# Kernel optimization log

Hardware: AMD Instinct MI355X
Metric: run time of the kernel (lower is better)

Reference implementation:

```python
import jax, jax.numpy as jnp
import numpy as np

B, N, T, E = 8, 4096, 16, 65536
D, H, O = 768, 4, 256
PER_TURN = N // T
NEG = -1e30


def setup_inputs() -> dict:
    key = jax.random.key(0)
    k = jax.random.split(key, 10)
    x = jax.random.normal(k[0], (B, N, D), dtype=jnp.float32)
    # turns sorted within each graph: node i has turn i // PER_TURN
    turns = jnp.tile(jnp.repeat(jnp.arange(T, dtype=jnp.int32), PER_TURN)[None, :], (B, 1))
    # edges: dst uniform over nodes, src uniform over nodes with turn[src] <= turn[dst]
    dst = jax.random.randint(k[1], (B, E), 0, N, dtype=jnp.int32)
    bound = (dst // PER_TURN + 1) * PER_TURN
    u = jax.random.uniform(k[2], (B, E), dtype=jnp.float32)
    src = jnp.minimum((u * bound).astype(jnp.int32), bound - 1)
    edge_index = jnp.stack([src, dst], axis=1)  # [B, 2, E]
    W = jax.random.normal(k[3], (D, H * D), dtype=jnp.float32) * 0.02
    a_src = jax.random.normal(k[4], (H, D), dtype=jnp.float32) * 0.05
    a_dst = jax.random.normal(k[5], (H, D), dtype=jnp.float32) * 0.05
    b_gat = jnp.zeros((D,), jnp.float32)
    w_att = jax.random.normal(k[6], (D, 1), dtype=jnp.float32) * 0.05
    b_att = jnp.zeros((1,), jnp.float32)
    w_cls = jax.random.normal(k[7], (D, O), dtype=jnp.float32) * 0.05
    b_cls = jnp.zeros((O,), jnp.float32)
    return dict(x=x, edge_index=edge_index, turns=turns, W=W, a_src=a_src,
                a_dst=a_dst, b_gat=b_gat, w_att=w_att, b_att=b_att,
                w_cls=w_cls, b_cls=b_cls)


def _forward(x, edge_index, turns, W, a_src, a_dst, b_gat, w_att, b_att, w_cls, b_cls, n_turns):
    n = x.shape[1]
    h_heads, d = a_src.shape

    def graph_fn(args):
        xg, ei, tg = args
        src, dst = ei[0], ei[1]

        def step(xc, t):
            active = tg <= t                                  # subgraph node mask [N]
            h = (xc @ W).reshape(n, h_heads, d)               # [N,H,D] per-head projections
            asrc = jnp.einsum('nhd,hd->nh', h, a_src)         # [N,H]
            adst = jnp.einsum('nhd,hd->nh', h, a_dst)
            emask = tg[dst] == t                              # only edges into current turn
            e = jax.nn.leaky_relu(asrc[src] + adst[dst], 0.2)  # [E,H]
            e = jnp.where(emask[:, None], e, NEG)
            # PyG GATConv add_self_loops=True: self-loop on every subgraph node
            s = jax.nn.leaky_relu(asrc + adst, 0.2)           # [N,H]
            s = jnp.where(active[:, None], s, NEG)
            m = jnp.maximum(jax.ops.segment_max(e, dst, num_segments=n), s)
            m = jnp.where(m > NEG * 0.5, m, 0.0)              # safe max for empty segments
            ee = jnp.where(emask[:, None], jnp.exp(e - m[dst]), 0.0)   # [E,H]
            se = jnp.where(active[:, None], jnp.exp(s - m), 0.0)       # [N,H]
            denom = jax.ops.segment_sum(ee, dst, num_segments=n) + se  # [N,H]
            msg = jax.ops.segment_sum(ee[:, :, None] * h[src], dst, num_segments=n)
            out = (msg + se[:, :, None] * h) / jnp.where(denom > 0, denom, 1.0)[:, :, None]
            out = out.mean(axis=1) + b_gat                    # concat=False -> mean over heads
            xn = jnp.where(active[:, None], out, xc)          # write back into graph.x
            # GlobalAttention pooling over subgraph nodes
            gate = (xn @ w_att + b_att).squeeze(-1)           # [N]
            g = jax.nn.softmax(jnp.where(active, gate, NEG))
            pooled = g @ xn                                   # [D]
            return xn, pooled @ w_cls + b_cls                 # [O]

        _, outs = jax.lax.scan(step, xg, jnp.arange(n_turns))
        return outs                                           # [T,O]

    outs = jax.lax.map(graph_fn, (x, edge_index, turns))      # sequential over graphs
    return outs[:, :, None, :]                                # [B,T,1,O] like torch.stack nesting


def reference(x, edge_index, turns, W, a_src, a_dst, b_gat, w_att, b_att, w_cls, b_cls):
    n_turns = int(turns.max()) + 1
    return _forward(x, edge_index, turns, W, a_src, a_dst, b_gat, w_att, b_att,
                    w_cls, b_cls, n_turns)
```

## Files before the change

kernel.cpp:

```cpp
#include <hip/hip_runtime.h>

typedef __attribute__((ext_vector_type(8))) short short8;
typedef __attribute__((ext_vector_type(8))) unsigned short ushort8;
typedef __attribute__((ext_vector_type(4))) float f32x4;

__device__ __forceinline__ float b2f(unsigned short u){
  union { unsigned int i; float f; } v; v.i = ((unsigned int)u)<<16; return v.f;
}
__device__ __forceinline__ unsigned short f2b(float f){
  unsigned int x = __float_as_uint(f);
  return (unsigned short)((x + 0x7fffu + ((x>>16)&1u))>>16);
}

__device__ __forceinline__ void gload16(const unsigned short* g, unsigned short* l){
  __builtin_amdgcn_global_load_lds((const __attribute__((address_space(1))) unsigned int*)g,
                                   (__attribute__((address_space(3))) unsigned int*)l, 16, 0, 0);
}

__global__ __launch_bounds__(256) void k_zero(int* p){
  p[blockIdx.x*256 + threadIdx.x] = 0;
}

__global__ __launch_bounds__(256) void k_hist(const int* __restrict__ ei, int* __restrict__ cnt){
  int idx = blockIdx.x*256 + threadIdx.x;
  int b = idx>>16, e = idx&65535;
  int dst = ei[b*131072 + 65536 + e];
  atomicAdd(&cnt[b*4096 + dst], 1);
}

__global__ __launch_bounds__(1024) void k_scan(int* __restrict__ cnt, int* __restrict__ offs){
  int b = blockIdx.x, tid = threadIdx.x;
  __shared__ int sums[1024];
  int base = tid*4;
  int c0 = cnt[b*4096+base+0], c1 = cnt[b*4096+base+1];
  int c2 = cnt[b*4096+base+2], c3 = cnt[b*4096+base+3];
  int t1 = c0, t2 = c0+c1, t3 = c0+c1+c2, tot = t3+c3;
  sums[tid] = tot;
  __syncthreads();
  for (int off=1; off<1024; off<<=1){
    int add = (tid>=off) ? sums[tid-off] : 0;
    __syncthreads();
    sums[tid] += add;
    __syncthreads();
  }
  int eb = sums[tid] - tot;
  offs[b*4097+base+0] = eb;      offs[b*4097+base+1] = eb+t1;
  offs[b*4097+base+2] = eb+t2;   offs[b*4097+base+3] = eb+t3;
  cnt[b*4096+base+0] = eb;       cnt[b*4096+base+1] = eb+t1;
  cnt[b*4096+base+2] = eb+t2;    cnt[b*4096+base+3] = eb+t3;
  if (tid==1023) offs[b*4097+4096] = sums[1023];
}

__global__ __launch_bounds__(256) void k_scatter(const int* __restrict__ ei, int* __restrict__ cur,
                                                 int* __restrict__ ss){
  int idx = blockIdx.x*256 + threadIdx.x;
  int b = idx>>16, e = idx&65535;
  int src = ei[b*131072 + e];
  int dst = ei[b*131072 + 65536 + e];
  int pos = atomicAdd(&cur[b*4096 + dst], 1);
  ss[b*65536 + pos] = src;
}

__global__ __launch_bounds__(256) void k_vavd(const float* __restrict__ W, const float* __restrict__ a_src,
                                              const float* __restrict__ a_dst, float* __restrict__ vavd){
  int wid = blockIdx.x*4 + (threadIdx.x>>6);
  int lane = threadIdx.x & 63;
  int i = wid>>3, h8 = wid&7, h = h8&3;
  const float* a = (h8<4 ? a_src : a_dst) + h*768;
  const float* wrow = W + i*3072 + h*768;
  float acc = 0.f;
  #pragma unroll
  for (int j12=0; j12<12; j12++){ int j = lane + j12*64; acc += wrow[j]*a[j]; }
  #pragma unroll
  for (int d=1; d<64; d<<=1) acc += __shfl_xor(acc, d);
  if (lane==0) vavd[i*8 + h8] = acc;
}

__global__ __launch_bounds__(256) void k_prep_w(const float* __restrict__ W, unsigned short* __restrict__ wmT,
                                                unsigned short* __restrict__ wpT){
  int g = blockIdx.x*256 + threadIdx.x;
  int i = g%768, j = g/768;
  float s = 0.f;
  #pragma unroll
  for (int h=0; h<4; h++){
    float w = W[i*3072 + h*768 + j];
    s += w;
    wpT[j*3072 + h*768 + i] = f2b(w);
  }
  wmT[j*768 + i] = f2b(0.25f*s);
}

__global__ __launch_bounds__(256) void k_prep0(const float* __restrict__ x0, const float* __restrict__ vavd,
                                               float* __restrict__ ad0){
  int b = blockIdx.y;
  int node = blockIdx.x*4 + (threadIdx.x>>6);
  int lane = threadIdx.x & 63;
  size_t roff = (size_t)(b*4096 + node)*768;
  float acc[8];
  #pragma unroll
  for (int k=0;k<8;k++) acc[k]=0.f;
  #pragma unroll
  for (int j12=0; j12<12; j12++){
    int j = lane + j12*64;
    float xv = x0[roff + j];
    const float* vp = vavd + j*8;
    #pragma unroll
    for (int k=0;k<8;k++) acc[k]+=xv*vp[k];
  }
  #pragma unroll
  for (int k=0;k<8;k++){
    #pragma unroll
    for (int d=1; d<64; d<<=1) acc[k] += __shfl_xor(acc[k], d);
  }
  if (lane==0){
    float* o = ad0 + (size_t)(b*4096 + node)*8;
    #pragma unroll
    for (int k=0;k<8;k++) o[k]=acc[k];
  }
}

__global__ __launch_bounds__(256) void k_edge(const float* __restrict__ x0, const unsigned short* __restrict__ stc,
                                              const float* __restrict__ ad, const float* __restrict__ ad0,
                                              const int* __restrict__ offs,
                                              const int* __restrict__ ssrc, unsigned short* __restrict__ zbuf, int t){
  int b = blockIdx.y, dl = blockIdx.x, tid = threadIdx.x;
  int dst = t*256 + dl;
  int lane = tid&63, wv = tid>>6;
  int e0 = offs[b*4097 + dst], e1 = offs[b*4097 + dst + 1];
  const float* adr = ad0 + (size_t)(b*4096 + dst)*8;
  float ad0_=adr[4], ad1_=adr[5], ad2_=adr[6], ad3_=adr[7];
  float sh[4];
  { float v;
    v=adr[0]+ad0_; sh[0]=v>0.f?v:0.2f*v;
    v=adr[1]+ad1_; sh[1]=v>0.f?v:0.2f*v;
    v=adr[2]+ad2_; sh[2]=v>0.f?v:0.2f*v;
    v=adr[3]+ad3_; sh[3]=v>0.f?v:0.2f*v; }
  int band = t*256;
  float mx[4] = {-1e30f,-1e30f,-1e30f,-1e30f};
  for (int i=e0+tid; i<e1; i+=256){
    int s = ssrc[b*65536 + i];
    const float* ap = (s >= band ? ad0 : ad) + (size_t)(b*4096 + s)*8;
    float v;
    v=ap[0]+ad0_; v=v>0.f?v:0.2f*v; mx[0]=fmaxf(mx[0],v);
    v=ap[1]+ad1_; v=v>0.f?v:0.2f*v; mx[1]=fmaxf(mx[1],v);
    v=ap[2]+ad2_; v=v>0.f?v:0.2f*v; mx[2]=fmaxf(mx[2],v);
    v=ap[3]+ad3_; v=v>0.f?v:0.2f*v; mx[3]=fmaxf(mx[3],v);
  }
  #pragma unroll
  for (int h=0;h<4;h++){
    #pragma unroll
    for (int d=1; d<64; d<<=1) mx[h] = fmaxf(mx[h], __shfl_xor(mx[h], d));
  }
  __shared__ float redm[4][4];
  if (lane==0){ redm[wv][0]=mx[0]; redm[wv][1]=mx[1]; redm[wv][2]=mx[2]; redm[wv][3]=mx[3]; }
  __syncthreads();
  float m[4];
  #pragma unroll
  for (int h=0;h<4;h++)
    m[h] = fmaxf(fmaxf(fmaxf(redm[0][h],redm[1][h]),fmaxf(redm[2][h],redm[3][h])), sh[h]);

  __shared__ float4 eeL[256];
  __shared__ int srcL[256];
  float den0=0.f,den1=0.f,den2=0.f,den3=0.f;
  float za[4][3] = {{0,0,0},{0,0,0},{0,0,0},{0,0,0}};
  for (int base=e0; base<e1; base+=256){
    __syncthreads();
    int i = base + tid;
    if (i < e1){
      int s = ssrc[b*65536 + i];
      const float* ap = (s >= band ? ad0 : ad) + (size_t)(b*4096 + s)*8;
      float4 wq; float v;
      v=ap[0]+ad0_; v=v>0.f?v:0.2f*v; wq.x=expf(v-m[0]); den0+=wq.x;
      v=ap[1]+ad1_; v=v>0.f?v:0.2f*v; wq.y=expf(v-m[1]); den1+=wq.y;
      v=ap[2]+ad2_; v=v>0.f?v:0.2f*v; wq.z=expf(v-m[2]); den2+=wq.z;
      v=ap[3]+ad3_; v=v>0.f?v:0.2f*v; wq.w=expf(v-m[3]); den3+=wq.w;
      eeL[tid] = wq; srcL[tid] = s;
    }
    __syncthreads();
    int cnt = e1 - base; if (cnt > 256) cnt = 256;
    for (int k=0; k<cnt; k++){
      float4 wq = eeL[k];
      int s = srcL[k];
      float xv0, xv1, xv2;
      if (s < band){
        const unsigned short* r = stc + (size_t)(b*4096 + s)*768;
        xv0=b2f(r[tid]); xv1=b2f(r[tid+256]); xv2=b2f(r[tid+512]);
      } else {
        const float* r = x0 + (size_t)(b*4096 + s)*768;
        xv0=r[tid]; xv1=r[tid+256]; xv2=r[tid+512];
      }
      za[0][0]+=wq.x*xv0; za[0][1]+=wq.x*xv1; za[0][2]+=wq.x*xv2;
      za[1][0]+=wq.y*xv0; za[1][1]+=wq.y*xv1; za[1][2]+=wq.y*xv2;
      za[2][0]+=wq.z*xv0; za[2][1]+=wq.z*xv1; za[2][2]+=wq.z*xv2;
      za[3][0]+=wq.w*xv0; za[3][1]+=wq.w*xv1; za[3][2]+=wq.w*xv2;
    }
  }
  float se[4];
  #pragma unroll
  for (int h=0;h<4;h++) se[h] = expf(sh[h]-m[h]);
  { const float* r = x0 + (size_t)(b*4096 + dst)*768;
    float xv0=r[tid], xv1=r[tid+256], xv2=r[tid+512];
    za[0][0]+=se[0]*xv0; za[0][1]+=se[0]*xv1; za[0][2]+=se[0]*xv2;
    za[1][0]+=se[1]*xv0; za[1][1]+=se[1]*xv1; za[1][2]+=se[1]*xv2;
    za[2][0]+=se[2]*xv0; za[2][1]+=se[2]*xv1; za[2][2]+=se[2]*xv2;
    za[3][0]+=se[3]*xv0; za[3][1]+=se[3]*xv1; za[3][2]+=se[3]*xv2; }
  float den[4]={den0,den1,den2,den3};
  #pragma unroll
  for (int h=0;h<4;h++){
    #pragma unroll
    for (int d=1; d<64; d<<=1) den[h] += __shfl_xor(den[h], d);
  }
  __shared__ float redd[4][4];
  if (lane==0){ redd[wv][0]=den[0]; redd[wv][1]=den[1]; redd[wv][2]=den[2]; redd[wv][3]=den[3]; }
  __syncthreads();
  unsigned short* zp = zbuf + (size_t)(b*256 + dl)*3072;
  #pragma unroll
  for (int h=0;h<4;h++){
    float dtot = redd[0][h]+redd[1][h]+redd[2][h]+redd[3][h] + se[h];
    float sc = 0.25f/dtot;
    zp[h*768 + tid      ] = f2b(za[h][0]*sc);
    zp[h*768 + tid + 256] = f2b(za[h][1]*sc);
    zp[h*768 + tid + 512] = f2b(za[h][2]*sc);
  }
}

__global__ __launch_bounds__(512) void k_mm(const unsigned short* __restrict__ zbuf,
                                            const unsigned short* __restrict__ wpT,
                                            const unsigned short* __restrict__ stc,
                                            const unsigned short* __restrict__ wmT,
                                            const float* __restrict__ bias,
                                            unsigned short* __restrict__ partA,
                                            unsigned short* __restrict__ stn, int t){
  int nwg = gridDim.x, orig = blockIdx.x;
  int cpx = nwg>>3;
  int j = (orig&7)*cpx + (orig>>3);

  int tid = threadIdx.x, lane = tid&63, w = tid>>6;
  bool jobA = j < 192;
  const unsigned short *Ap, *Bp;
  int lda, ldb, s = 0, b = 0, mrow, ncol;
  if (jobA){
    s = j/48; int q = j%48;
    mrow = (q/6)*256; ncol = (q%6)*128;
    Ap = zbuf + (size_t)mrow*3072 + s*768;  lda = 3072;
    Bp = wpT  + (size_t)ncol*3072 + s*768;  ldb = 3072;
  } else {
    int idx = j - 192; int pg = 6*t;
    b = idx/pg; int rr = idx%pg;
    mrow = (rr/6)*256; ncol = (rr%6)*128;
    Ap = stc + (size_t)b*4096*768 + (size_t)mrow*768;  lda = 768;
    Bp = wmT + (size_t)ncol*768;                       ldb = 768;
  }
  int wr = (w>>1)*64, wc = (w&1)*64;
  int lrow = lane&15, lk = (lane>>4)*8;
  __shared__ unsigned short As[3][256*32];
  __shared__ unsigned short Bs[3][128*32];
  f32x4 acc[4][4];
  #pragma unroll
  for (int m=0;m<4;m++)
    #pragma unroll
    for (int n2=0;n2<4;n2++) acc[m][n2] = (f32x4){0.f,0.f,0.f,0.f};
  int srow = w*16 + (lane>>2);
  int skb  = (lane&3)*8;
  const unsigned short* ga0 = Ap + (size_t)srow*lda + skb;
  const unsigned short* ga1 = Ap + (size_t)(128+srow)*lda + skb;
  const unsigned short* gb0 = Bp + (size_t)srow*ldb + skb;
  int lo = w*512;
  #define STAGE(bi) { gload16(ga0, &As[bi][lo]); gload16(ga1, &As[bi][4096+lo]); \
                      gload16(gb0, &Bs[bi][lo]); \
                      ga0 += 32; ga1 += 32; gb0 += 32; }
  STAGE(0)
  STAGE(1)
  #pragma unroll
  for (int kt=0; kt<24; kt++){
    int cur = kt%3;
    if (kt < 22) STAGE((kt+2)%3)
    if (kt < 22)      asm volatile("s_waitcnt vmcnt(6)" ::: "memory");
    else if (kt==22)  asm volatile("s_waitcnt vmcnt(3)" ::: "memory");
    else              asm volatile("s_waitcnt vmcnt(0)" ::: "memory");
    __builtin_amdgcn_sched_barrier(0);
    __builtin_amdgcn_s_barrier();
    __builtin_amdgcn_sched_barrier(0);
    short8 af[4], bf[4];
    #pragma unroll
    for (int m=0;m<4;m++)  af[m]  = *(const short8*)&As[cur][(wr + m*16 + lrow)*32 + lk];
    #pragma unroll
    for (int n2=0;n2<4;n2++) bf[n2] = *(const short8*)&Bs[cur][(wc + n2*16 + lrow)*32 + lk];
    __builtin_amdgcn_s_setprio(1);
    #pragma unroll
    for (int m=0;m<4;m++)
      #pragma unroll
      for (int n2=0;n2<4;n2++)
        acc[m][n2] = __builtin_amdgcn_mfma_f32_16x16x32_bf16(af[m], bf[n2], acc[m][n2], 0,0,0);
    __builtin_amdgcn_s_setprio(0);
    __builtin_amdgcn_sched_barrier(0);
    __builtin_amdgcn_s_barrier();
    __builtin_amdgcn_sched_barrier(0);
  }
  #undef STAGE
  if (jobA){
    unsigned short* op = partA + (size_t)s*2048*768;
    #pragma unroll
    for (int m=0;m<4;m++)
      #pragma unroll
      for (int n2=0;n2<4;n2++)
        #pragma unroll
        for (int r=0;r<4;r++){
          int gr = mrow + wr + m*16 + (lane>>4)*4 + r;
          int gc = ncol + wc + n2*16 + (lane&15);
          op[(size_t)gr*768 + gc] = f2b(acc[m][n2][r]);
        }
  } else {
    unsigned short* cp = stn + (size_t)b*4096*768;
    #pragma unroll
    for (int m=0;m<4;m++)
      #pragma unroll
      for (int n2=0;n2<4;n2++)
        #pragma unroll
        for (int r=0;r<4;r++){
          int gr = mrow + wr + m*16 + (lane>>4)*4 + r;
          int gc = ncol + wc + n2*16 + (lane&15);
          cp[(size_t)gr*768 + gc] = f2b(acc[m][n2][r] + bias[gc]);
        }
  }
}

__global__ __launch_bounds__(256) void k_post(const unsigned short* __restrict__ partA, const float* __restrict__ bias,
                                              const float* __restrict__ vavd, const float* __restrict__ w_att,
                                              const unsigned short* __restrict__ st,
                                              unsigned short* __restrict__ stn, float* __restrict__ ad,
                                              float* __restrict__ gate, int t){
  int j = blockIdx.x, tid = threadIdx.x;
  int lane = tid&63, wv = tid>>6;
  if (j < 2048){
    int r = j;
    int g = r>>8;
    size_t e = (size_t)r*768;
    const size_t SL = (size_t)2048*768;
    int c0 = tid, c1 = tid+256, c2 = tid+512;
    float v0 = b2f(partA[e+c0]) + b2f(partA[SL+e+c0]) + b2f(partA[2*SL+e+c0]) + b2f(partA[3*SL+e+c0]) + bias[c0];
    float v1 = b2f(partA[e+c1]) + b2f(partA[SL+e+c1]) + b2f(partA[2*SL+e+c1]) + b2f(partA[3*SL+e+c1]) + bias[c1];
    float v2 = b2f(partA[e+c2]) + b2f(partA[SL+e+c2]) + b2f(partA[2*SL+e+c2]) + b2f(partA[3*SL+e+c2]) + bias[c2];
    size_t ro = ((size_t)g*4096 + t*256 + (r&255))*768;
    stn[ro+c0] = f2b(v0); stn[ro+c1] = f2b(v1); stn[ro+c2] = f2b(v2);
    float acc[9];
    const float *p0 = vavd + c0*8, *p1 = vavd + c1*8, *p2 = vavd + c2*8;
    #pragma unroll
    for (int k=0;k<8;k++) acc[k] = v0*p0[k] + v1*p1[k] + v2*p2[k];
    acc[8] = v0*w_att[c0] + v1*w_att[c1] + v2*w_att[c2];
    #pragma unroll
    for (int k=0;k<9;k++){
      #pragma unroll
      for (int d=1; d<64; d<<=1) acc[k] += __shfl_xor(acc[k], d);
    }
    __shared__ float red[4][9];
    if (lane==0){
      #pragma unroll
      for (int k=0;k<9;k++) red[wv][k]=acc[k];
    }
    __syncthreads();
    if (tid==0){
      size_t no = (size_t)g*4096 + t*256 + (r&255);
      float* o = ad + no*8;
      #pragma unroll
      for (int k=0;k<8;k++) o[k] = red[0][k]+red[1][k]+red[2][k]+red[3][k];
      gate[no] = red[0][8]+red[1][8]+red[2][8]+red[3][8];
    }
  } else {
    int idx = j - 2048;
    int per = t*64;
    int b = idx/per;
    int node = (idx%per)*4 + (tid>>6);
    size_t roff = (size_t)(b*4096 + node)*768;
    float acc[9];
    #pragma unroll
    for (int k=0;k<9;k++) acc[k]=0.f;
    #pragma unroll
    for (int j12=0; j12<12; j12++){
      int jj = lane + j12*64;
      float xv = b2f(st[roff + jj]);
      const float* vp = vavd + jj*8;
      acc[0]+=xv*vp[0]; acc[1]+=xv*vp[1]; acc[2]+=xv*vp[2]; acc[3]+=xv*vp[3];
      acc[4]+=xv*vp[4]; acc[5]+=xv*vp[5]; acc[6]+=xv*vp[6]; acc[7]+=xv*vp[7];
      acc[8]+=xv*w_att[jj];
    }
    #pragma unroll
    for (int k=0;k<9;k++){
      #pragma unroll
      for (int d=1; d<64; d<<=1) acc[k] += __shfl_xor(acc[k], d);
    }
    if (lane==0){
      float* o = ad + (size_t)(b*4096 + node)*8;
      #pragma unroll
      for (int k=0;k<8;k++) o[k]=acc[k];
      gate[b*4096 + node] = acc[8];
    }
  }
}

__global__ __launch_bounds__(256) void k_pool(const unsigned short* __restrict__ st, const float* __restrict__ gate,
                                              float* __restrict__ part, int t){
  int b = blockIdx.y, bx = blockIdx.x, tid = threadIdx.x;
  int lane = tid&63, wv = tid>>6;
  int A = (t+1)*256;
  const float* g = gate + b*4096;
  float mx = -1e30f;
  for (int i=tid; i<A; i+=256) mx = fmaxf(mx, g[i]);
  #pragma unroll
  for (int d=1; d<64; d<<=1) mx = fmaxf(mx, __shfl_xor(mx, d));
  __shared__ float rm[4];
  if (lane==0) rm[wv]=mx;
  __syncthreads();
  mx = fmaxf(fmaxf(rm[0],rm[1]), fmaxf(rm[2],rm[3]));
  float s = 0.f;
  for (int i=tid; i<A; i+=256) s += expf(g[i]-mx);
  #pragma unroll
  for (int d=1; d<64; d<<=1) s += __shfl_xor(s, d);
  __shared__ float rs[4];
  if (lane==0) rs[wv]=s;
  __syncthreads();
  float invS = 1.f/(rs[0]+rs[1]+rs[2]+rs[3]);
  int slice = A>>5;
  int n0 = bx*slice;
  float a0=0.f, a1=0.f, a2=0.f;
  for (int n=n0; n<n0+slice; n++){
    float wgt = expf(g[n]-mx)*invS;
    const unsigned short* r = st + (size_t)(b*4096 + n)*768;
    a0 += wgt*b2f(r[tid]); a1 += wgt*b2f(r[tid+256]); a2 += wgt*b2f(r[tid+512]);
  }
  float* p = part + (size_t)(b*32 + bx)*768;
  p[tid]=a0; p[tid+256]=a1; p[tid+512]=a2;
}

__global__ __launch_bounds__(256) void k_cls(const float* __restrict__ part, const float* __restrict__ w_cls,
                                             const float* __restrict__ b_cls, float* __restrict__ out, int t){
  int b = blockIdx.x, cg = blockIdx.y, tid = threadIdx.x;
  __shared__ float pooled[768];
  #pragma unroll
  for (int cc=0; cc<3; cc++){
    float s=0.f; int jj = tid + cc*256;
    for (int p=0; p<32; p++) s += part[(size_t)(b*32+p)*768 + jj];
    pooled[jj] = s;
  }
  __syncthreads();
  int col = tid&31, sub = tid>>5;
  int gcol = cg*32 + col;
  float s = 0.f;
  for (int jj=sub*96; jj<sub*96+96; jj++) s += pooled[jj]*w_cls[jj*256 + gcol];
  __shared__ float red[8][32];
  red[sub][col] = s;
  __syncthreads();
  if (tid < 32){
    float acc = b_cls[cg*32+tid];
    #pragma unroll
    for (int k=0;k<8;k++) acc += red[k][tid];
    out[b*4096 + t*256 + cg*32 + tid] = acc;
  }
}

extern "C" void kernel_launch(void* const* d_in, const int* in_sizes, int n_in,
                              void* d_out, int out_size, void* d_ws, size_t ws_size,
                              hipStream_t stream){
  const float* x0    = (const float*)d_in[0];
  const int*   ei    = (const int*)d_in[1];
  const float* W     = (const float*)d_in[3];
  const float* a_src = (const float*)d_in[4];
  const float* a_dst = (const float*)d_in[5];
  const float* b_gat = (const float*)d_in[6];
  const float* w_att = (const float*)d_in[7];
  const float* w_cls = (const float*)d_in[9];
  const float* b_cls = (const float*)d_in[10];
  float* out = (float*)d_out;
  char* ws = (char*)d_ws;

  size_t pos = 0;
  auto alloc = [&](size_t sz)->char*{ char* r = ws + pos; pos = (pos + sz + 255) & ~(size_t)255; return r; };
  unsigned short* st0  = (unsigned short*)alloc((size_t)8*4096*768*2);
  unsigned short* st1  = (unsigned short*)alloc((size_t)8*4096*768*2);
  unsigned short* zbuf = (unsigned short*)alloc((size_t)8*256*3072*2);
  float* adbuf = (float*)alloc((size_t)8*4096*8*4);
  float* ad0   = (float*)alloc((size_t)8*4096*8*4);
  float* gate  = (float*)alloc((size_t)8*4096*4);
  int*   ssrc  = (int*)alloc((size_t)8*65536*4);
  int*   offs  = (int*)alloc((size_t)8*4097*4);
  int*   curs  = (int*)alloc((size_t)8*4096*4);
  float* vavd  = (float*)alloc((size_t)768*8*4);
  unsigned short* wm = (unsigned short*)alloc((size_t)768*768*2);
  unsigned short* wp = (unsigned short*)alloc((size_t)768*3072*2);
  float* part  = (float*)alloc((size_t)8*32*768*4);
  unsigned short* partA = (unsigned short*)alloc((size_t)4*2048*768*2);
  unsigned short* st[2] = {st0, st1};

  k_zero   <<<128, 256, 0, stream>>>(curs);
  k_hist   <<<2048, 256, 0, stream>>>(ei, curs);
  k_scan   <<<8, 1024, 0, stream>>>(curs, offs);
  k_scatter<<<2048, 256, 0, stream>>>(ei, curs, ssrc);
  k_vavd   <<<1536, 256, 0, stream>>>(W, a_src, a_dst, vavd);
  k_prep_w <<<2304, 256, 0, stream>>>(W, wm, wp);
  k_prep0  <<<dim3(1024,8), 256, 0, stream>>>(x0, vavd, ad0);

  for (int t=0; t<16; t++){
    int cur = t&1, nxt = cur^1;
    k_edge<<<dim3(256,8), 256, 0, stream>>>(x0, st[cur], adbuf, ad0, offs, ssrc, zbuf, t);
    k_mm <<<192 + 48*t, 512, 0, stream>>>(zbuf, wp, st[cur], wm, b_gat, partA, st[nxt], t);
    k_post<<<2048 + t*512, 256, 0, stream>>>(partA, b_gat, vavd, w_att, st[nxt], st[nxt], adbuf, gate, t);
    k_pool<<<dim3(32,8), 256, 0, stream>>>(st[nxt], gate, part, t);
    k_cls <<<dim3(8,8), 256, 0, stream>>>(part, w_cls, b_cls, out, t);
  }
}
```

Before: 1.878 ms.

## Fuse pooling and classifier into next turn's edge kernel; single-barrier GEMM pipeline

The pooling for turn t-1 now runs as extra blocks inside the edge kernel of turn t, and the classifier is folded into the last pooling block per graph through an atomic counter. This removes two kernel launches per turn and lets pooling overlap with edge work, with one trailing launch handling the final turn. The GEMM main loop also moves the next-stage prefetch after the barrier and drops the second barrier per k-step, relaxing the wait count. In exchange it adds a threadfence/atomic last-block pattern and a serial 768-length classifier dot product per thread.

New measurement: 2.397 ms. +27.6%, slower.

```diff
diff --git a/kernel.cpp b/kernel.cpp
--- a/kernel.cpp
+++ b/kernel.cpp
@@ -119,13 +119,68 @@
   }
 }
 
-__global__ __launch_bounds__(256) void k_edge(const float* __restrict__ x0, const unsigned short* __restrict__ stc,
-                                              const float* __restrict__ ad, const float* __restrict__ ad0,
-                                              const int* __restrict__ offs,
-                                              const int* __restrict__ ssrc, unsigned short* __restrict__ zbuf, int t){
-  int b = blockIdx.y, dl = blockIdx.x, tid = threadIdx.x;
+__global__ __launch_bounds__(256) void k_edgepool(const float* __restrict__ x0, const unsigned short* __restrict__ stc,
+                                                  const float* __restrict__ ad, const float* __restrict__ ad0,
+                                                  const int* __restrict__ offs, const int* __restrict__ ssrc,
+                                                  unsigned short* __restrict__ zbuf, int t,
+                                                  const unsigned short* __restrict__ stp, const float* __restrict__ gate,
+                                                  float* __restrict__ part, const float* __restrict__ w_cls,
+                                                  const float* __restrict__ b_cls, float* __restrict__ out,
+                                                  int* __restrict__ pcnt, int pool_t, int edge_blocks){
+  int bx = blockIdx.x, b = blockIdx.y, tid = threadIdx.x;
+  int lane = tid&63, wv = tid>>6;
+  if (bx >= edge_blocks){
+    int slice_i = bx - edge_blocks;
+    int A = (pool_t+1)*256;
+    const float* g = gate + b*4096;
+    float mx = -1e30f;
+    for (int i=tid; i<A; i+=256) mx = fmaxf(mx, g[i]);
+    #pragma unroll
+    for (int d=1; d<64; d<<=1) mx = fmaxf(mx, __shfl_xor(mx, d));
+    __shared__ float rm[4];
+    if (lane==0) rm[wv]=mx;
+    __syncthreads();
+    mx = fmaxf(fmaxf(rm[0],rm[1]), fmaxf(rm[2],rm[3]));
+    float s = 0.f;
+    for (int i=tid; i<A; i+=256) s += expf(g[i]-mx);
+    #pragma unroll
+    for (int d=1; d<64; d<<=1) s += __shfl_xor(s, d);
+    __shared__ float rs[4];
+    if (lane==0) rs[wv]=s;
+    __syncthreads();
+    float invS = 1.f/(rs[0]+rs[1]+rs[2]+rs[3]);
+    int slice = A>>5;
+    int n0 = slice_i*slice;
+    float a0=0.f, a1=0.f, a2=0.f;
+    for (int n=n0; n<n0+slice; n++){
+      float wgt = expf(g[n]-mx)*invS;
+      const unsigned short* r = stp + (size_t)(b*4096 + n)*768;
+      a0 += wgt*b2f(r[tid]); a1 += wgt*b2f(r[tid+256]); a2 += wgt*b2f(r[tid+512]);
+    }
+    float* p = part + (size_t)(b*32 + slice_i)*768;
+    p[tid]=a0; p[tid+256]=a1; p[tid+512]=a2;
+    __shared__ int lastflag;
+    __threadfence();
+    if (tid==0){ int old = atomicAdd(&pcnt[b], 1); lastflag = (old==31); }
+    __syncthreads();
+    if (!lastflag) return;
+    __threadfence();
+    __shared__ float pooled[768];
+    #pragma unroll
+    for (int cc=0; cc<3; cc++){
+      float ps=0.f; int jj = tid + cc*256;
+      for (int pp=0; pp<32; pp++) ps += part[(size_t)(b*32+pp)*768 + jj];
+      pooled[jj] = ps;
+    }
+    __syncthreads();
+    float acc2 = b_cls[tid];
+    for (int jj=0; jj<768; jj++) acc2 += pooled[jj]*w_cls[jj*256 + tid];
+    out[b*4096 + pool_t*256 + tid] = acc2;
+    if (tid==0) pcnt[b] = 0;
+    return;
+  }
+  int dl = bx;
   int dst = t*256 + dl;
-  int lane = tid&63, wv = tid>>6;
   int e0 = offs[b*4097 + dst], e1 = offs[b*4097 + dst + 1];
   const float* adr = ad0 + (size_t)(b*4096 + dst)*8;
   float ad0_=adr[4], ad1_=adr[5], ad2_=adr[6], ad3_=adr[7];
@@ -274,13 +329,12 @@
   #pragma unroll
   for (int kt=0; kt<24; kt++){
     int cur = kt%3;
-    if (kt < 22) STAGE((kt+2)%3)
-    if (kt < 22)      asm volatile("s_waitcnt vmcnt(6)" ::: "memory");
-    else if (kt==22)  asm volatile("s_waitcnt vmcnt(3)" ::: "memory");
-    else              asm volatile("s_waitcnt vmcnt(0)" ::: "memory");
+    if (kt < 23) asm volatile("s_waitcnt vmcnt(3)" ::: "memory");
+    else         asm volatile("s_waitcnt vmcnt(0)" ::: "memory");
     __builtin_amdgcn_sched_barrier(0);
     __builtin_amdgcn_s_barrier();
     __builtin_amdgcn_sched_barrier(0);
+    if (kt < 22) STAGE((kt+2)%3)
     short8 af[4], bf[4];
     #pragma unroll
     for (int m=0;m<4;m++)  af[m]  = *(const short8*)&As[cur][(wr + m*16 + lrow)*32 + lk];
@@ -293,9 +347,6 @@
       for (int n2=0;n2<4;n2++)
         acc[m][n2] = __builtin_amdgcn_mfma_f32_16x16x32_bf16(af[m], bf[n2], acc[m][n2], 0,0,0);
     __builtin_amdgcn_s_setprio(0);
-    __builtin_amdgcn_sched_barrier(0);
-    __builtin_amdgcn_s_barrier();
-    __builtin_amdgcn_sched_barrier(0);
   }
   #undef STAGE
   if (jobA){
@@ -398,66 +449,6 @@
   }
 }
 
-__global__ __launch_bounds__(256) void k_pool(const unsigned short* __restrict__ st, const float* __restrict__ gate,
-                                              float* __restrict__ part, int t){
-  int b = blockIdx.y, bx = blockIdx.x, tid = threadIdx.x;
-  int lane = tid&63, wv = tid>>6;
-  int A = (t+1)*256;
-  const float* g = gate + b*4096;
-  float mx = -1e30f;
-  for (int i=tid; i<A; i+=256) mx = fmaxf(mx, g[i]);
-  #pragma unroll
-  for (int d=1; d<64; d<<=1) mx = fmaxf(mx, __shfl_xor(mx, d));
-  __shared__ float rm[4];
-  if (lane==0) rm[wv]=mx;
-  __syncthreads();
-  mx = fmaxf(fmaxf(rm[0],rm[1]), fmaxf(rm[2],rm[3]));
-  float s = 0.f;
-  for (int i=tid; i<A; i+=256) s += expf(g[i]-mx);
-  #pragma unroll
-  for (int d=1; d<64; d<<=1) s += __shfl_xor(s, d);
-  __shared__ float rs[4];
-  if (lane==0) rs[wv]=s;
-  __syncthreads();
-  float invS = 1.f/(rs[0]+rs[1]+rs[2]+rs[3]);
-  int slice = A>>5;
-  int n0 = bx*slice;
-  float a0=0.f, a1=0.f, a2=0.f;
-  for (int n=n0; n<n0+slice; n++){
-    float wgt = expf(g[n]-mx)*invS;
-    const unsigned short* r = st + (size_t)(b*4096 + n)*768;
-    a0 += wgt*b2f(r[tid]); a1 += wgt*b2f(r[tid+256]); a2 += wgt*b2f(r[tid+512]);
-  }
-  float* p = part + (size_t)(b*32 + bx)*768;
-  p[tid]=a0; p[tid+256]=a1; p[tid+512]=a2;
-}
-
-__global__ __launch_bounds__(256) void k_cls(const float* __restrict__ part, const float* __restrict__ w_cls,
-                                             const float* __restrict__ b_cls, float* __restrict__ out, int t){
-  int b = blockIdx.x, cg = blockIdx.y, tid = threadIdx.x;
-  __shared__ float pooled[768];
-  #pragma unroll
-  for (int cc=0; cc<3; cc++){
-    float s=0.f; int jj = tid + cc*256;
-    for (int p=0; p<32; p++) s += part[(size_t)(b*32+p)*768 + jj];
-    pooled[jj] = s;
-  }
-  __syncthreads();
-  int col = tid&31, sub = tid>>5;
-  int gcol = cg*32 + col;
-  float s = 0.f;
-  for (int jj=sub*96; jj<sub*96+96; jj++) s += pooled[jj]*w_cls[jj*256 + gcol];
-  __shared__ float red[8][32];
-  red[sub][col] = s;
-  __syncthreads();
-  if (tid < 32){
-    float acc = b_cls[cg*32+tid];
-    #pragma unroll
-    for (int k=0;k<8;k++) acc += red[k][tid];
-    out[b*4096 + t*256 + cg*32 + tid] = acc;
-  }
-}
-
 extern "C" void kernel_launch(void* const* d_in, const int* in_sizes, int n_in,
                               void* d_out, int out_size, void* d_ws, size_t ws_size,
                               hipStream_t stream){
@@ -489,9 +480,11 @@
   unsigned short* wp = (unsigned short*)alloc((size_t)768*3072*2);
   float* part  = (float*)alloc((size_t)8*32*768*4);
   unsigned short* partA = (unsigned short*)alloc((size_t)4*2048*768*2);
+  int*   pcnt  = (int*)alloc((size_t)256*4);
   unsigned short* st[2] = {st0, st1};
 
   k_zero   <<<128, 256, 0, stream>>>(curs);
+  k_zero   <<<1, 256, 0, stream>>>(pcnt);
   k_hist   <<<2048, 256, 0, stream>>>(ei, curs);
   k_scan   <<<8, 1024, 0, stream>>>(curs, offs);
   k_scatter<<<2048, 256, 0, stream>>>(ei, curs, ssrc);
@@ -501,10 +494,13 @@
 
   for (int t=0; t<16; t++){
     int cur = t&1, nxt = cur^1;
-    k_edge<<<dim3(256,8), 256, 0, stream>>>(x0, st[cur], adbuf, ad0, offs, ssrc, zbuf, t);
+    int ebl = 256;
+    int gx = (t==0) ? 256 : 288;
+    k_edgepool<<<dim3(gx,8), 256, 0, stream>>>(x0, st[cur], adbuf, ad0, offs, ssrc, zbuf, t,
+                                               st[cur], gate, part, w_cls, b_cls, out, pcnt, t-1, ebl);
     k_mm <<<192 + 48*t, 512, 0, stream>>>(zbuf, wp, st[cur], wm, b_gat, partA, st[nxt], t);
     k_post<<<2048 + t*512, 256, 0, stream>>>(partA, b_gat, vavd, w_att, st[nxt], st[nxt], adbuf, gate, t);
-    k_pool<<<dim3(32,8), 256, 0, stream>>>(st[nxt], gate, part, t);
-    k_cls <<<dim3(8,8), 256, 0, stream>>>(part, w_cls, b_cls, out, t);
-  }
-}
+  }
+  k_edgepool<<<dim3(32,8), 256, 0, stream>>>(x0, st[0], adbuf, ad0, offs, ssrc, zbuf, 15,
+                                             st[0], gate, part, w_cls, b_cls, out, pcnt, 15, 0);
+}
```
